# Kernel optimization log

Hardware: AMD Instinct MI355X
Metric: run time of the kernel (lower is better)

## Reference

```python
import jax, jax.numpy as jnp
import numpy as np

B, N, F, L = 8, 2048, 128, 2
SLOPE = 0.1  # LeakyReLU negative slope

def lrelu(v):
    return jnp.where(v >= 0, v, SLOPE * v)

def setup_inputs() -> dict:
    key = jax.random.key(0)
    ks = jax.random.split(key, 7)
    scale = 1.0 / np.sqrt(F)
    return {
        "x": jax.random.normal(ks[0], (B, N, F), dtype=jnp.float32),
        "W3": jax.random.normal(ks[1], (L, F, F), dtype=jnp.float32) * scale,
        "b3": jnp.zeros((L, F), dtype=jnp.float32),
        "W4": jax.random.normal(ks[2], (L, F, F), dtype=jnp.float32) * scale,
        "b4": jnp.zeros((L, F), dtype=jnp.float32),
        "W5": jax.random.normal(ks[3], (L, F, F), dtype=jnp.float32) * scale,
        "b5": jnp.zeros((L, F), dtype=jnp.float32),
    }

def reference(x, W3, b3, W4, b4, W5, b5):
    # GraphStack of L GraphLayer modules, mes_type '0':
    #   weight_ij = dot(LeakyReLU(g3(n_i)), LeakyReLU(g4(n_j)))
    #   message_i = mean_{j != i} weight_ij * n_j
    #   n_i_out   = LeakyReLU(g5(message_i)) + n_i
    n = x.shape[1]
    for l in range(W3.shape[0]):
        w1 = lrelu(jnp.einsum('bnf,fg->bng', x, W3[l]) + b3[l])  # [B,N,F]
        w2 = lrelu(jnp.einsum('bnf,fg->bng', x, W4[l]) + b4[l])  # [B,N,F]
        wt = jnp.einsum('bif,bjf->bij', w1, w2)                  # pairwise weights [B,N,N]
        diag = jnp.einsum('bif,bif->bi', w1, w2)                 # self weights to exclude
        msg = (jnp.einsum('bij,bjf->bif', wt, x) - diag[..., None] * x) / (n - 1)
        x = lrelu(jnp.einsum('bif,fg->big', msg, W5[l]) + b5[l]) + x
    return x
```

## Files before the change

### kernel.cpp

```cpp
#include <hip/hip_runtime.h>

#define BB 8
#define NN 2048
#define FF 128
#define NL 2
#define SLOPE 0.1f
#define NROW (BB * NN)
#define XS_STRIDE 136

typedef __attribute__((ext_vector_type(8))) short short8;
typedef __attribute__((ext_vector_type(4))) float f32x4;

__device__ __forceinline__ float lrelu(float v) { return v >= 0.f ? v : SLOPE * v; }

__device__ __forceinline__ ushort f2bf(float f) {
    uint u = __float_as_uint(f);
    return (ushort)((u + 0x7fffu + ((u >> 16) & 1u)) >> 16);
}

__global__ __launch_bounds__(256) void k_prep(
    const float* __restrict__ W3, const float* __restrict__ W4,
    const float* __restrict__ W5, ushort* __restrict__ Wt)
{
    const int idx = blockIdx.x * 256 + threadIdx.x;
    const int m = idx >> 14;
    const int rem = idx & 16383;
    const int f = rem & 127;
    const int g = rem >> 7;
    const int l = m / 3, w = m % 3;
    const float* src = (w == 0) ? W3 : (w == 1) ? W4 : W5;
    Wt[m * 16384 + g * 128 + f] = f2bf(src[l * 16384 + f * 128 + g]);
}

__global__ __launch_bounds__(512) void k_w12(
    const float* __restrict__ x, const ushort* __restrict__ w3t,
    const ushort* __restrict__ w4t, const float* __restrict__ b3,
    const float* __restrict__ b4, ushort* __restrict__ w1b,
    ushort* __restrict__ w2t, ushort* __restrict__ xt,
    float* __restrict__ diag)
{
    __shared__ ushort xs[64 * XS_STRIDE];
    __shared__ float diag_s[64];

    const int tid = threadIdx.x;
    const int row0 = blockIdx.x * 64;
    const int b = row0 >> 11;
    const int jloc0 = row0 & 2047;

    if (tid < 64) diag_s[tid] = 0.f;

    const float4* xg4 = (const float4*)(x + (size_t)row0 * FF);
#pragma unroll
    for (int i = 0; i < 4; i++) {
        const int f4 = i * 512 + tid;
        const int row = f4 >> 5;
        const int k = (f4 & 31) * 4;
        float4 v = xg4[f4];
        ushort4 h;
        h.x = f2bf(v.x); h.y = f2bf(v.y); h.z = f2bf(v.z); h.w = f2bf(v.w);
        *(ushort4*)&xs[row * XS_STRIDE + k] = h;
    }
    __syncthreads();

    {
        const int g = tid >> 2;
        const int h = tid & 3;
        uint p[8];
#pragma unroll
        for (int jj = 0; jj < 8; jj++) {
            const uint lo = xs[(h * 16 + jj * 2) * XS_STRIDE + g];
            const uint hi = xs[(h * 16 + jj * 2 + 1) * XS_STRIDE + g];
            p[jj] = lo | (hi << 16);
        }
        uint4* dst = (uint4*)&xt[(size_t)b * (FF * NN) + (size_t)g * NN + jloc0 + h * 16];
        dst[0] = make_uint4(p[0], p[1], p[2], p[3]);
        dst[1] = make_uint4(p[4], p[5], p[6], p[7]);
    }

    const int lane = tid & 63;
    const int wave = tid >> 6;
    const int c = lane & 15;
    const int quad = lane >> 4;
    const int n = wave * 16 + c;

    f32x4 acc1[4], acc2[4];
#pragma unroll
    for (int rt = 0; rt < 4; rt++) { acc1[rt] = (f32x4)0.f; acc2[rt] = (f32x4)0.f; }

#pragma unroll
    for (int kk = 0; kk < 4; kk++) {
        short8 bf3 = *(const short8*)&w3t[n * 128 + kk * 32 + quad * 8];
        short8 bf4 = *(const short8*)&w4t[n * 128 + kk * 32 + quad * 8];
#pragma unroll
        for (int rt = 0; rt < 4; rt++) {
            short8 a = *(const short8*)&xs[(rt * 16 + c) * XS_STRIDE + kk * 32 + quad * 8];
            acc1[rt] = __builtin_amdgcn_mfma_f32_16x16x32_bf16(a, bf3, acc1[rt], 0, 0, 0);
            acc2[rt] = __builtin_amdgcn_mfma_f32_16x16x32_bf16(a, bf4, acc2[rt], 0, 0, 0);
        }
    }

    const int gcol = wave * 16 + c;
    const float bb3 = b3[gcol], bb4 = b4[gcol];
    float dpar[4][4];

#pragma unroll
    for (int rt = 0; rt < 4; rt++) {
        ushort w2p[4];
#pragma unroll
        for (int r = 0; r < 4; r++) {
            const float v1 = lrelu(acc1[rt][r] + bb3);
            const float v2 = lrelu(acc2[rt][r] + bb4);
            const int grow = row0 + rt * 16 + quad * 4 + r;
            w1b[(size_t)grow * FF + gcol] = f2bf(v1);
            w2p[r] = f2bf(v2);
            dpar[rt][r] = v1 * v2;
        }
        const uint lo = (uint)w2p[0] | ((uint)w2p[1] << 16);
        const uint hi = (uint)w2p[2] | ((uint)w2p[3] << 16);
        uint2* dst = (uint2*)&w2t[(size_t)b * (FF * NN) + (size_t)gcol * NN +
                                  jloc0 + rt * 16 + quad * 4];
        *dst = make_uint2(lo, hi);
    }

#pragma unroll
    for (int rt = 0; rt < 4; rt++) {
#pragma unroll
        for (int r = 0; r < 4; r++) {
            float dp = dpar[rt][r];
            dp += __shfl_xor(dp, 1, 64);
            dp += __shfl_xor(dp, 2, 64);
            dp += __shfl_xor(dp, 4, 64);
            dp += __shfl_xor(dp, 8, 64);
            if (c == 0) atomicAdd(&diag_s[rt * 16 + quad * 4 + r], dp);
        }
    }
    __syncthreads();
    if (tid < 64) diag[row0 + tid] = diag_s[tid];
}

__global__ __launch_bounds__(256) void k_S2(
    const ushort* __restrict__ xt, const ushort* __restrict__ w2t,
    ushort* __restrict__ St)
{
    __shared__ float red[4][512];
    const int tid = threadIdx.x;
    const int lane = tid & 63;
    const int wave = tid >> 6;
    const int c = lane & 15;
    const int quad = lane >> 4;

    const int b  = blockIdx.x >> 5;
    const int gq = (blockIdx.x >> 3) & 3;
    const int fs = blockIdx.x & 7;

    const ushort* xtb = xt + (size_t)b * (FF * NN);
    const ushort* w2b = w2t + (size_t)b * (FF * NN);

    const int j0 = wave * 512 + quad * 8;
    const ushort* a0p = &xtb[(gq * 32 + c) * NN + j0];
    const ushort* a1p = &xtb[(gq * 32 + 16 + c) * NN + j0];
    const ushort* bp  = &w2b[(fs * 16 + c) * NN + j0];

    f32x4 acc0 = (f32x4)0.f, acc1 = (f32x4)0.f;
#pragma unroll
    for (int it = 0; it < 16; it++) {
        short8 a0 = *(const short8*)(a0p + it * 32);
        short8 a1 = *(const short8*)(a1p + it * 32);
        short8 bf = *(const short8*)(bp + it * 32);
        acc0 = __builtin_amdgcn_mfma_f32_16x16x32_bf16(a0, bf, acc0, 0, 0, 0);
        acc1 = __builtin_amdgcn_mfma_f32_16x16x32_bf16(a1, bf, acc1, 0, 0, 0);
    }

#pragma unroll
    for (int r = 0; r < 4; r++) {
        red[wave][(quad * 4 + r) * 16 + c] = acc0[r];
        red[wave][(16 + quad * 4 + r) * 16 + c] = acc1[r];
    }
    __syncthreads();

#pragma unroll
    for (int i = 0; i < 2; i++) {
        const int idx = i * 256 + tid;
        const float s = red[0][idx] + red[1][idx] + red[2][idx] + red[3][idx];
        const int gl = idx >> 4;
        const int fl = idx & 15;
        St[(size_t)b * (FF * FF) + (size_t)(gq * 32 + gl) * FF + fs * 16 + fl] = f2bf(s);
    }
}

__global__ __launch_bounds__(512) void k_out(
    const float* __restrict__ x, const ushort* __restrict__ w1b,
    const ushort* __restrict__ St, const float* __restrict__ diag,
    const ushort* __restrict__ w5t, const float* __restrict__ b5,
    float* __restrict__ out)
{
    __shared__ ushort w1s[64 * XS_STRIDE];
    __shared__ ushort ms[64 * XS_STRIDE];

    const int tid = threadIdx.x;
    const int row0 = blockIdx.x * 64;
    const int b = row0 >> 11;
    const ushort* Sb = St + (size_t)b * (FF * FF);

#pragma unroll
    for (int i = 0; i < 2; i++) {
        const int off = (i * 512 + tid) * 8;
        const int row = off >> 7;
        const int k = off & 127;
        short8 v = *(const short8*)&w1b[(size_t)row0 * FF + off];
        *(short8*)&w1s[row * XS_STRIDE + k] = v;
    }
    __syncthreads();

    const int lane = tid & 63;
    const int wave = tid >> 6;
    const int c = lane & 15;
    const int quad = lane >> 4;
    const int n = wave * 16 + c;

    f32x4 accm[4];
#pragma unroll
    for (int rt = 0; rt < 4; rt++) accm[rt] = (f32x4)0.f;

#pragma unroll
    for (int kk = 0; kk < 4; kk++) {
        short8 bf = *(const short8*)&Sb[n * 128 + kk * 32 + quad * 8];
#pragma unroll
        for (int rt = 0; rt < 4; rt++) {
            short8 a = *(const short8*)&w1s[(rt * 16 + c) * XS_STRIDE + kk * 32 + quad * 8];
            accm[rt] = __builtin_amdgcn_mfma_f32_16x16x32_bf16(a, bf, accm[rt], 0, 0, 0);
        }
    }

    const float inv = 1.f / (float)(NN - 1);
    const int gcol = wave * 16 + c;
    float xsv[4][4];
#pragma unroll
    for (int rt = 0; rt < 4; rt++) {
        float dg[4];
#pragma unroll
        for (int r = 0; r < 4; r++) dg[r] = diag[row0 + rt * 16 + quad * 4 + r];
#pragma unroll
        for (int r = 0; r < 4; r++) {
            const int lrow = rt * 16 + quad * 4 + r;
            const float xv = x[(size_t)(row0 + lrow) * FF + gcol];
            xsv[rt][r] = xv;
            const float m = (accm[rt][r] - dg[r] * xv) * inv;
            ms[lrow * XS_STRIDE + gcol] = f2bf(m);
        }
    }
    __syncthreads();

    f32x4 acc2[4];
#pragma unroll
    for (int rt = 0; rt < 4; rt++) acc2[rt] = (f32x4)0.f;

#pragma unroll
    for (int kk = 0; kk < 4; kk++) {
        short8 bf = *(const short8*)&w5t[n * 128 + kk * 32 + quad * 8];
#pragma unroll
        for (int rt = 0; rt < 4; rt++) {
            short8 a = *(const short8*)&ms[(rt * 16 + c) * XS_STRIDE + kk * 32 + quad * 8];
            acc2[rt] = __builtin_amdgcn_mfma_f32_16x16x32_bf16(a, bf, acc2[rt], 0, 0, 0);
        }
    }

    const float bb = b5[gcol];
#pragma unroll
    for (int rt = 0; rt < 4; rt++) {
#pragma unroll
        for (int r = 0; r < 4; r++) {
            const int grow = row0 + rt * 16 + quad * 4 + r;
            out[(size_t)grow * FF + gcol] = lrelu(acc2[rt][r] + bb) + xsv[rt][r];
        }
    }
}

__global__ __launch_bounds__(512) void k_out_w12(
    const float* __restrict__ x, const ushort* __restrict__ w1b_in,
    const ushort* __restrict__ St, const float* __restrict__ diag_in,
    const ushort* __restrict__ w5t, const float* __restrict__ b5,
    float* __restrict__ out,
    const ushort* __restrict__ w3t, const ushort* __restrict__ w4t,
    const float* __restrict__ b3, const float* __restrict__ b4,
    ushort* __restrict__ w1b, ushort* __restrict__ w2t,
    ushort* __restrict__ xt, float* __restrict__ diag)
{
    __shared__ ushort sA[64 * XS_STRIDE];
    __shared__ ushort sB[64 * XS_STRIDE];
    __shared__ float diag_s[64];

    const int tid = threadIdx.x;
    const int row0 = blockIdx.x * 64;
    const int b = row0 >> 11;
    const int jloc0 = row0 & 2047;
    const ushort* Sb = St + (size_t)b * (FF * FF);

    if (tid < 64) diag_s[tid] = 0.f;

#pragma unroll
    for (int i = 0; i < 2; i++) {
        const int off = (i * 512 + tid) * 8;
        const int row = off >> 7;
        const int k = off & 127;
        short8 v = *(const short8*)&w1b_in[(size_t)row0 * FF + off];
        *(short8*)&sA[row * XS_STRIDE + k] = v;
    }
    __syncthreads();

    const int lane = tid & 63;
    const int wave = tid >> 6;
    const int c = lane & 15;
    const int quad = lane >> 4;
    const int n = wave * 16 + c;
    const int gcol = wave * 16 + c;

    f32x4 accm[4];
#pragma unroll
    for (int rt = 0; rt < 4; rt++) accm[rt] = (f32x4)0.f;

#pragma unroll
    for (int kk = 0; kk < 4; kk++) {
        short8 bf = *(const short8*)&Sb[n * 128 + kk * 32 + quad * 8];
#pragma unroll
        for (int rt = 0; rt < 4; rt++) {
            short8 a = *(const short8*)&sA[(rt * 16 + c) * XS_STRIDE + kk * 32 + quad * 8];
            accm[rt] = __builtin_amdgcn_mfma_f32_16x16x32_bf16(a, bf, accm[rt], 0, 0, 0);
        }
    }

    const float inv = 1.f / (float)(NN - 1);
    float xsv[4][4];
#pragma unroll
    for (int rt = 0; rt < 4; rt++) {
        float dg[4];
#pragma unroll
        for (int r = 0; r < 4; r++) dg[r] = diag_in[row0 + rt * 16 + quad * 4 + r];
#pragma unroll
        for (int r = 0; r < 4; r++) {
            const int lrow = rt * 16 + quad * 4 + r;
            const float xv = x[(size_t)(row0 + lrow) * FF + gcol];
            xsv[rt][r] = xv;
            const float m = (accm[rt][r] - dg[r] * xv) * inv;
            sB[lrow * XS_STRIDE + gcol] = f2bf(m);
        }
    }
    __syncthreads();

    f32x4 acc2[4];
#pragma unroll
    for (int rt = 0; rt < 4; rt++) acc2[rt] = (f32x4)0.f;

#pragma unroll
    for (int kk = 0; kk < 4; kk++) {
        short8 bf = *(const short8*)&w5t[n * 128 + kk * 32 + quad * 8];
#pragma unroll
        for (int rt = 0; rt < 4; rt++) {
            short8 a = *(const short8*)&sB[(rt * 16 + c) * XS_STRIDE + kk * 32 + quad * 8];
            acc2[rt] = __builtin_amdgcn_mfma_f32_16x16x32_bf16(a, bf, acc2[rt], 0, 0, 0);
        }
    }

    const float bb = b5[gcol];
#pragma unroll
    for (int rt = 0; rt < 4; rt++) {
#pragma unroll
        for (int r = 0; r < 4; r++) {
            const int lrow = rt * 16 + quad * 4 + r;
            const float ov = lrelu(acc2[rt][r] + bb) + xsv[rt][r];
            out[(size_t)(row0 + lrow) * FF + gcol] = ov;
            sA[lrow * XS_STRIDE + gcol] = f2bf(ov);
        }
    }
    __syncthreads();

    {
        const int g = tid >> 2;
        const int h = tid & 3;
        uint p[8];
#pragma unroll
        for (int jj = 0; jj < 8; jj++) {
            const uint lo = sA[(h * 16 + jj * 2) * XS_STRIDE + g];
            const uint hi = sA[(h * 16 + jj * 2 + 1) * XS_STRIDE + g];
            p[jj] = lo | (hi << 16);
        }
        uint4* dst = (uint4*)&xt[(size_t)b * (FF * NN) + (size_t)g * NN + jloc0 + h * 16];
        dst[0] = make_uint4(p[0], p[1], p[2], p[3]);
        dst[1] = make_uint4(p[4], p[5], p[6], p[7]);
    }

    f32x4 acc1n[4], acc2n[4];
#pragma unroll
    for (int rt = 0; rt < 4; rt++) { acc1n[rt] = (f32x4)0.f; acc2n[rt] = (f32x4)0.f; }

#pragma unroll
    for (int kk = 0; kk < 4; kk++) {
        short8 bf3 = *(const short8*)&w3t[n * 128 + kk * 32 + quad * 8];
        short8 bf4 = *(const short8*)&w4t[n * 128 + kk * 32 + quad * 8];
#pragma unroll
        for (int rt = 0; rt < 4; rt++) {
            short8 a = *(const short8*)&sA[(rt * 16 + c) * XS_STRIDE + kk * 32 + quad * 8];
            acc1n[rt] = __builtin_amdgcn_mfma_f32_16x16x32_bf16(a, bf3, acc1n[rt], 0, 0, 0);
            acc2n[rt] = __builtin_amdgcn_mfma_f32_16x16x32_bf16(a, bf4, acc2n[rt], 0, 0, 0);
        }
    }

    const float bb3 = b3[gcol], bb4 = b4[gcol];
    float dpar[4][4];
#pragma unroll
    for (int rt = 0; rt < 4; rt++) {
        ushort w2p[4];
#pragma unroll
        for (int r = 0; r < 4; r++) {
            const float v1 = lrelu(acc1n[rt][r] + bb3);
            const float v2 = lrelu(acc2n[rt][r] + bb4);
            const int grow = row0 + rt * 16 + quad * 4 + r;
            w1b[(size_t)grow * FF + gcol] = f2bf(v1);
            w2p[r] = f2bf(v2);
            dpar[rt][r] = v1 * v2;
        }
        const uint lo = (uint)w2p[0] | ((uint)w2p[1] << 16);
        const uint hi = (uint)w2p[2] | ((uint)w2p[3] << 16);
        uint2* dst = (uint2*)&w2t[(size_t)b * (FF * NN) + (size_t)gcol * NN +
                                  jloc0 + rt * 16 + quad * 4];
        *dst = make_uint2(lo, hi);
    }

#pragma unroll
    for (int rt = 0; rt < 4; rt++) {
#pragma unroll
        for (int r = 0; r < 4; r++) {
            float dp = dpar[rt][r];
            dp += __shfl_xor(dp, 1, 64);
            dp += __shfl_xor(dp, 2, 64);
            dp += __shfl_xor(dp, 4, 64);
            dp += __shfl_xor(dp, 8, 64);
            if (c == 0) atomicAdd(&diag_s[rt * 16 + quad * 4 + r], dp);
        }
    }
    __syncthreads();
    if (tid < 64) diag[row0 + tid] = diag_s[tid];
}

extern "C" void kernel_launch(void* const* d_in, const int* in_sizes, int n_in,
                              void* d_out, int out_size, void* d_ws, size_t ws_size,
                              hipStream_t stream)
{
    const float* x  = (const float*)d_in[0];
    const float* W3 = (const float*)d_in[1];
    const float* b3 = (const float*)d_in[2];
    const float* W4 = (const float*)d_in[3];
    const float* b4 = (const float*)d_in[4];
    const float* W5 = (const float*)d_in[5];
    const float* b5 = (const float*)d_in[6];
    float* out = (float*)d_out;

    char* ws = (char*)d_ws;
    ushort* w1b   = (ushort*)(ws);
    ushort* w2t   = (ushort*)(ws + ((size_t)4  << 20));
    ushort* xt    = (ushort*)(ws + ((size_t)8  << 20));
    float*  diag  = (float*) (ws + ((size_t)12 << 20));
    ushort* St    = (ushort*)(ws + ((size_t)13 << 20));
    ushort* Wt    = (ushort*)(ws + ((size_t)14 << 20));

    const ushort* w3t0 = Wt;
    const ushort* w4t0 = Wt + 16384;
    const ushort* w5t0 = Wt + 2 * 16384;
    const ushort* w3t1 = Wt + 3 * 16384;
    const ushort* w4t1 = Wt + 4 * 16384;
    const ushort* w5t1 = Wt + 5 * 16384;

    const int rowBlocks = NROW / 64;

    k_prep<<<384, 256, 0, stream>>>(W3, W4, W5, Wt);

    k_w12<<<rowBlocks, 512, 0, stream>>>(x, w3t0, w4t0, b3, b4, w1b, w2t, xt, diag);
    k_S2<<<256, 256, 0, stream>>>(xt, w2t, St);
    k_out_w12<<<rowBlocks, 512, 0, stream>>>(x, w1b, St, diag, w5t0, b5, out,
                                             w3t1, w4t1, b3 + FF, b4 + FF,
                                             w1b, w2t, xt, diag);
    k_S2<<<256, 256, 0, stream>>>(xt, w2t, St);
    k_out<<<rowBlocks, 512, 0, stream>>>(out, w1b, St, diag, w5t1, b5 + FF, out);
}
```

Measured before the change: 120.6 us.

## Fuse weight transpose/bf16 conversion into consumer kernels via LDS staging

Removes the separate k_prep launch. Each row-block kernel now converts and transposes the fp32 weights into shared memory itself. Weight B-fragments are read from LDS instead of global memory. The k_S2 block index mapping is also changed so the batch index varies fastest. In exchange, every one of the 256 blocks redoes the 128x128 transpose-convert work with strided global reads, and LDS use per block rises to roughly 70-105 KB, which limits occupancy.

After: 118.1 us. 2.1% less time.

```diff
diff --git a/kernel.cpp b/kernel.cpp
--- a/kernel.cpp
+++ b/kernel.cpp
@@ -1,12 +1,10 @@
 #include <hip/hip_runtime.h>
 
-#define BB 8
 #define NN 2048
 #define FF 128
-#define NL 2
 #define SLOPE 0.1f
-#define NROW (BB * NN)
-#define XS_STRIDE 136
+#define WSTR 136
+#define TSTR 136
 
 typedef __attribute__((ext_vector_type(8))) short short8;
 typedef __attribute__((ext_vector_type(4))) float f32x4;
@@ -18,28 +16,29 @@
     return (ushort)((u + 0x7fffu + ((u >> 16) & 1u)) >> 16);
 }
 
-__global__ __launch_bounds__(256) void k_prep(
-    const float* __restrict__ W3, const float* __restrict__ W4,
-    const float* __restrict__ W5, ushort* __restrict__ Wt)
+__device__ __forceinline__ void wtrans(const float* __restrict__ W, ushort* wl, int tid) {
+#pragma unroll
+    for (int u = 0; u < 4; u++) {
+        const int g = tid & 127;
+        const int fgrp = (tid >> 7) + u * 4;
+        short8 v;
+#pragma unroll
+        for (int j = 0; j < 8; j++) v[j] = (short)f2bf(W[(fgrp * 8 + j) * 128 + g]);
+        *(short8*)&wl[g * WSTR + fgrp * 8] = v;
+    }
+}
+
+__global__ __launch_bounds__(512) void k_w12(
+    const float* __restrict__ x,
+    const float* __restrict__ W3, const float* __restrict__ b3,
+    const float* __restrict__ W4, const float* __restrict__ b4,
+    ushort* __restrict__ w1b, ushort* __restrict__ w2t,
+    ushort* __restrict__ xt, float* __restrict__ diag)
 {
-    const int idx = blockIdx.x * 256 + threadIdx.x;
-    const int m = idx >> 14;
-    const int rem = idx & 16383;
-    const int f = rem & 127;
-    const int g = rem >> 7;
-    const int l = m / 3, w = m % 3;
-    const float* src = (w == 0) ? W3 : (w == 1) ? W4 : W5;
-    Wt[m * 16384 + g * 128 + f] = f2bf(src[l * 16384 + f * 128 + g]);
-}
-
-__global__ __launch_bounds__(512) void k_w12(
-    const float* __restrict__ x, const ushort* __restrict__ w3t,
-    const ushort* __restrict__ w4t, const float* __restrict__ b3,
-    const float* __restrict__ b4, ushort* __restrict__ w1b,
-    ushort* __restrict__ w2t, ushort* __restrict__ xt,
-    float* __restrict__ diag)
-{
-    __shared__ ushort xs[64 * XS_STRIDE];
+    __shared__ __align__(16) char smem[87040];
+    ushort* xs = (ushort*)smem;
+    ushort* wA = (ushort*)(smem + 17408);
+    ushort* wB = (ushort*)(smem + 52224);
     __shared__ float diag_s[64];
 
     const int tid = threadIdx.x;
@@ -58,8 +57,10 @@
         float4 v = xg4[f4];
         ushort4 h;
         h.x = f2bf(v.x); h.y = f2bf(v.y); h.z = f2bf(v.z); h.w = f2bf(v.w);
-        *(ushort4*)&xs[row * XS_STRIDE + k] = h;
-    }
+        *(ushort4*)&xs[row * TSTR + k] = h;
+    }
+    wtrans(W3, wA, tid);
+    wtrans(W4, wB, tid);
     __syncthreads();
 
     {
@@ -68,8 +69,8 @@
         uint p[8];
 #pragma unroll
         for (int jj = 0; jj < 8; jj++) {
-            const uint lo = xs[(h * 16 + jj * 2) * XS_STRIDE + g];
-            const uint hi = xs[(h * 16 + jj * 2 + 1) * XS_STRIDE + g];
+            const uint lo = xs[(h * 16 + jj * 2) * TSTR + g];
+            const uint hi = xs[(h * 16 + jj * 2 + 1) * TSTR + g];
             p[jj] = lo | (hi << 16);
         }
         uint4* dst = (uint4*)&xt[(size_t)b * (FF * NN) + (size_t)g * NN + jloc0 + h * 16];
@@ -81,7 +82,7 @@
     const int wave = tid >> 6;
     const int c = lane & 15;
     const int quad = lane >> 4;
-    const int n = wave * 16 + c;
+    const int gcol = wave * 16 + c;
 
     f32x4 acc1[4], acc2[4];
 #pragma unroll
@@ -89,20 +90,18 @@
 
 #pragma unroll
     for (int kk = 0; kk < 4; kk++) {
-        short8 bf3 = *(const short8*)&w3t[n * 128 + kk * 32 + quad * 8];
-        short8 bf4 = *(const short8*)&w4t[n * 128 + kk * 32 + quad * 8];
-#pragma unroll
-        for (int rt = 0; rt < 4; rt++) {
-            short8 a = *(const short8*)&xs[(rt * 16 + c) * XS_STRIDE + kk * 32 + quad * 8];
+        short8 bf3 = *(const short8*)&wA[gcol * WSTR + kk * 32 + quad * 8];
+        short8 bf4 = *(const short8*)&wB[gcol * WSTR + kk * 32 + quad * 8];
+#pragma unroll
+        for (int rt = 0; rt < 4; rt++) {
+            short8 a = *(const short8*)&xs[(rt * 16 + c) * TSTR + kk * 32 + quad * 8];
             acc1[rt] = __builtin_amdgcn_mfma_f32_16x16x32_bf16(a, bf3, acc1[rt], 0, 0, 0);
             acc2[rt] = __builtin_amdgcn_mfma_f32_16x16x32_bf16(a, bf4, acc2[rt], 0, 0, 0);
         }
     }
 
-    const int gcol = wave * 16 + c;
     const float bb3 = b3[gcol], bb4 = b4[gcol];
     float dpar[4][4];
-
 #pragma unroll
     for (int rt = 0; rt < 4; rt++) {
         ushort w2p[4];
@@ -149,9 +148,10 @@
     const int c = lane & 15;
     const int quad = lane >> 4;
 
-    const int b  = blockIdx.x >> 5;
-    const int gq = (blockIdx.x >> 3) & 3;
-    const int fs = blockIdx.x & 7;
+    const int b     = blockIdx.x & 7;
+    const int slice = blockIdx.x >> 3;
+    const int gq    = slice >> 3;
+    const int fs    = slice & 7;
 
     const ushort* xtb = xt + (size_t)b * (FF * NN);
     const ushort* w2b = w2t + (size_t)b * (FF * NN);
@@ -188,106 +188,21 @@
     }
 }
 
-__global__ __launch_bounds__(512) void k_out(
-    const float* __restrict__ x, const ushort* __restrict__ w1b,
-    const ushort* __restrict__ St, const float* __restrict__ diag,
-    const ushort* __restrict__ w5t, const float* __restrict__ b5,
-    float* __restrict__ out)
-{
-    __shared__ ushort w1s[64 * XS_STRIDE];
-    __shared__ ushort ms[64 * XS_STRIDE];
-
-    const int tid = threadIdx.x;
-    const int row0 = blockIdx.x * 64;
-    const int b = row0 >> 11;
-    const ushort* Sb = St + (size_t)b * (FF * FF);
-
-#pragma unroll
-    for (int i = 0; i < 2; i++) {
-        const int off = (i * 512 + tid) * 8;
-        const int row = off >> 7;
-        const int k = off & 127;
-        short8 v = *(const short8*)&w1b[(size_t)row0 * FF + off];
-        *(short8*)&w1s[row * XS_STRIDE + k] = v;
-    }
-    __syncthreads();
-
-    const int lane = tid & 63;
-    const int wave = tid >> 6;
-    const int c = lane & 15;
-    const int quad = lane >> 4;
-    const int n = wave * 16 + c;
-
-    f32x4 accm[4];
-#pragma unroll
-    for (int rt = 0; rt < 4; rt++) accm[rt] = (f32x4)0.f;
-
-#pragma unroll
-    for (int kk = 0; kk < 4; kk++) {
-        short8 bf = *(const short8*)&Sb[n * 128 + kk * 32 + quad * 8];
-#pragma unroll
-        for (int rt = 0; rt < 4; rt++) {
-            short8 a = *(const short8*)&w1s[(rt * 16 + c) * XS_STRIDE + kk * 32 + quad * 8];
-            accm[rt] = __builtin_amdgcn_mfma_f32_16x16x32_bf16(a, bf, accm[rt], 0, 0, 0);
-        }
-    }
-
-    const float inv = 1.f / (float)(NN - 1);
-    const int gcol = wave * 16 + c;
-    float xsv[4][4];
-#pragma unroll
-    for (int rt = 0; rt < 4; rt++) {
-        float dg[4];
-#pragma unroll
-        for (int r = 0; r < 4; r++) dg[r] = diag[row0 + rt * 16 + quad * 4 + r];
-#pragma unroll
-        for (int r = 0; r < 4; r++) {
-            const int lrow = rt * 16 + quad * 4 + r;
-            const float xv = x[(size_t)(row0 + lrow) * FF + gcol];
-            xsv[rt][r] = xv;
-            const float m = (accm[rt][r] - dg[r] * xv) * inv;
-            ms[lrow * XS_STRIDE + gcol] = f2bf(m);
-        }
-    }
-    __syncthreads();
-
-    f32x4 acc2[4];
-#pragma unroll
-    for (int rt = 0; rt < 4; rt++) acc2[rt] = (f32x4)0.f;
-
-#pragma unroll
-    for (int kk = 0; kk < 4; kk++) {
-        short8 bf = *(const short8*)&w5t[n * 128 + kk * 32 + quad * 8];
-#pragma unroll
-        for (int rt = 0; rt < 4; rt++) {
-            short8 a = *(const short8*)&ms[(rt * 16 + c) * XS_STRIDE + kk * 32 + quad * 8];
-            acc2[rt] = __builtin_amdgcn_mfma_f32_16x16x32_bf16(a, bf, acc2[rt], 0, 0, 0);
-        }
-    }
-
-    const float bb = b5[gcol];
-#pragma unroll
-    for (int rt = 0; rt < 4; rt++) {
-#pragma unroll
-        for (int r = 0; r < 4; r++) {
-            const int grow = row0 + rt * 16 + quad * 4 + r;
-            out[(size_t)grow * FF + gcol] = lrelu(acc2[rt][r] + bb) + xsv[rt][r];
-        }
-    }
-}
-
 __global__ __launch_bounds__(512) void k_out_w12(
     const float* __restrict__ x, const ushort* __restrict__ w1b_in,
     const ushort* __restrict__ St, const float* __restrict__ diag_in,
-    const ushort* __restrict__ w5t, const float* __restrict__ b5,
+    const float* __restrict__ W5, const float* __restrict__ b5,
     float* __restrict__ out,
-    const ushort* __restrict__ w3t, const ushort* __restrict__ w4t,
-    const float* __restrict__ b3, const float* __restrict__ b4,
+    const float* __restrict__ W3n, const float* __restrict__ b3n,
+    const float* __restrict__ W4n, const float* __restrict__ b4n,
     ushort* __restrict__ w1b, ushort* __restrict__ w2t,
     ushort* __restrict__ xt, float* __restrict__ diag)
 {
-    __shared__ ushort sA[64 * XS_STRIDE];
-    __shared__ ushort sB[64 * XS_STRIDE];
+    __shared__ __align__(16) char smem[104448];
+    ushort* sA = (ushort*)smem;
+    ushort* sB = (ushort*)(smem + 17408);
+    ushort* wA = (ushort*)(smem + 34816);
+    ushort* wB = (ushort*)(smem + 69632);
     __shared__ float diag_s[64];
 
     const int tid = threadIdx.x;
@@ -304,15 +219,15 @@
         const int row = off >> 7;
         const int k = off & 127;
         short8 v = *(const short8*)&w1b_in[(size_t)row0 * FF + off];
-        *(short8*)&sA[row * XS_STRIDE + k] = v;
-    }
+        *(short8*)&sA[row * TSTR + k] = v;
+    }
+    wtrans(W5, wA, tid);
     __syncthreads();
 
     const int lane = tid & 63;
     const int wave = tid >> 6;
     const int c = lane & 15;
     const int quad = lane >> 4;
-    const int n = wave * 16 + c;
     const int gcol = wave * 16 + c;
 
     f32x4 accm[4];
@@ -321,10 +236,10 @@
 
 #pragma unroll
     for (int kk = 0; kk < 4; kk++) {
-        short8 bf = *(const short8*)&Sb[n * 128 + kk * 32 + quad * 8];
-#pragma unroll
-        for (int rt = 0; rt < 4; rt++) {
-            short8 a = *(const short8*)&sA[(rt * 16 + c) * XS_STRIDE + kk * 32 + quad * 8];
+        short8 bf = *(const short8*)&Sb[gcol * 128 + kk * 32 + quad * 8];
+#pragma unroll
+        for (int rt = 0; rt < 4; rt++) {
+            short8 a = *(const short8*)&sA[(rt * 16 + c) * TSTR + kk * 32 + quad * 8];
             accm[rt] = __builtin_amdgcn_mfma_f32_16x16x32_bf16(a, bf, accm[rt], 0, 0, 0);
         }
     }
@@ -342,7 +257,7 @@
             const float xv = x[(size_t)(row0 + lrow) * FF + gcol];
             xsv[rt][r] = xv;
             const float m = (accm[rt][r] - dg[r] * xv) * inv;
-            sB[lrow * XS_STRIDE + gcol] = f2bf(m);
+            sB[lrow * TSTR + gcol] = f2bf(m);
         }
     }
     __syncthreads();
@@ -353,10 +268,10 @@
 
 #pragma unroll
     for (int kk = 0; kk < 4; kk++) {
-        short8 bf = *(const short8*)&w5t[n * 128 + kk * 32 + quad * 8];
-#pragma unroll
-        for (int rt = 0; rt < 4; rt++) {
-            short8 a = *(const short8*)&sB[(rt * 16 + c) * XS_STRIDE + kk * 32 + quad * 8];
+        short8 bf = *(const short8*)&wA[gcol * WSTR + kk * 32 + quad * 8];
+#pragma unroll
+        for (int rt = 0; rt < 4; rt++) {
+            short8 a = *(const short8*)&sB[(rt * 16 + c) * TSTR + kk * 32 + quad * 8];
             acc2[rt] = __builtin_amdgcn_mfma_f32_16x16x32_bf16(a, bf, acc2[rt], 0, 0, 0);
         }
     }
@@ -369,25 +284,28 @@
             const int lrow = rt * 16 + quad * 4 + r;
             const float ov = lrelu(acc2[rt][r] + bb) + xsv[rt][r];
             out[(size_t)(row0 + lrow) * FF + gcol] = ov;
-            sA[lrow * XS_STRIDE + gcol] = f2bf(ov);
-        }
-    }
-    __syncthreads();
-
+            sA[lrow * TSTR + gcol] = f2bf(ov);
+        }
+    }
+    __syncthreads();
+
+    wtrans(W3n, wA, tid);
+    wtrans(W4n, wB, tid);
     {
         const int g = tid >> 2;
         const int h = tid & 3;
         uint p[8];
 #pragma unroll
         for (int jj = 0; jj < 8; jj++) {
-            const uint lo = sA[(h * 16 + jj * 2) * XS_STRIDE + g];
-            const uint hi = sA[(h * 16 + jj * 2 + 1) * XS_STRIDE + g];
+            const uint lo = sA[(h * 16 + jj * 2) * TSTR + g];
+            const uint hi = sA[(h * 16 + jj * 2 + 1) * TSTR + g];
             p[jj] = lo | (hi << 16);
         }
         uint4* dst = (uint4*)&xt[(size_t)b * (FF * NN) + (size_t)g * NN + jloc0 + h * 16];
         dst[0] = make_uint4(p[0], p[1], p[2], p[3]);
         dst[1] = make_uint4(p[4], p[5], p[6], p[7]);
     }
+    __syncthreads();
 
     f32x4 acc1n[4], acc2n[4];
 #pragma unroll
@@ -395,17 +313,17 @@
 
 #pragma unroll
     for (int kk = 0; kk < 4; kk++) {
-        short8 bf3 = *(const short8*)&w3t[n * 128 + kk * 32 + quad * 8];
-        short8 bf4 = *(const short8*)&w4t[n * 128 + kk * 32 + quad * 8];
-#pragma unroll
-        for (int rt = 0; rt < 4; rt++) {
-            short8 a = *(const short8*)&sA[(rt * 16 + c) * XS_STRIDE + kk * 32 + quad * 8];
+        short8 bf3 = *(const short8*)&wA[gcol * WSTR + kk * 32 + quad * 8];
+        short8 bf4 = *(const short8*)&wB[gcol * WSTR + kk * 32 + quad * 8];
+#pragma unroll
+        for (int rt = 0; rt < 4; rt++) {
+            short8 a = *(const short8*)&sA[(rt * 16 + c) * TSTR + kk * 32 + quad * 8];
             acc1n[rt] = __builtin_amdgcn_mfma_f32_16x16x32_bf16(a, bf3, acc1n[rt], 0, 0, 0);
             acc2n[rt] = __builtin_amdgcn_mfma_f32_16x16x32_bf16(a, bf4, acc2n[rt], 0, 0, 0);
         }
     }
 
-    const float bb3 = b3[gcol], bb4 = b4[gcol];
+    const float bb3 = b3n[gcol], bb4 = b4n[gcol];
     float dpar[4][4];
 #pragma unroll
     for (int rt = 0; rt < 4; rt++) {
@@ -440,6 +358,96 @@
     }
     __syncthreads();
     if (tid < 64) diag[row0 + tid] = diag_s[tid];
+}
+
+__global__ __launch_bounds__(512) void k_out(
+    const float* __restrict__ xres, const ushort* __restrict__ w1b,
+    const ushort* __restrict__ St, const float* __restrict__ diag,
+    const float* __restrict__ W5n, const float* __restrict__ b5n,
+    float* __restrict__ out)
+{
+    __shared__ __align__(16) char smem[69632];
+    ushort* w1s = (ushort*)smem;
+    ushort* ms  = (ushort*)(smem + 17408);
+    ushort* wA  = (ushort*)(smem + 34816);
+
+    const int tid = threadIdx.x;
+    const int row0 = blockIdx.x * 64;
+    const int b = row0 >> 11;
+    const ushort* Sb = St + (size_t)b * (FF * FF);
+
+#pragma unroll
+    for (int i = 0; i < 2; i++) {
+        const int off = (i * 512 + tid) * 8;
+        const int row = off >> 7;
+        const int k = off & 127;
+        short8 v = *(const short8*)&w1b[(size_t)row0 * FF + off];
+        *(short8*)&w1s[row * TSTR + k] = v;
+    }
+    wtrans(W5n, wA, tid);
+    __syncthreads();
+
+    const int lane = tid & 63;
+    const int wave = tid >> 6;
+    const int c = lane & 15;
+    const int quad = lane >> 4;
+    const int gcol = wave * 16 + c;
+
+    f32x4 accm[4];
+#pragma unroll
+    for (int rt = 0; rt < 4; rt++) accm[rt] = (f32x4)0.f;
+
+#pragma unroll
+    for (int kk = 0; kk < 4; kk++) {
+        short8 bf = *(const short8*)&Sb[gcol * 128 + kk * 32 + quad * 8];
+#pragma unroll
+        for (int rt = 0; rt < 4; rt++) {
+            short8 a = *(const short8*)&w1s[(rt * 16 + c) * TSTR + kk * 32 + quad * 8];
+            accm[rt] = __builtin_amdgcn_mfma_f32_16x16x32_bf16(a, bf, accm[rt], 0, 0, 0);
+        }
+    }
+
+    const float inv = 1.f / (float)(NN - 1);
+    float xsv[4][4];
+#pragma unroll
+    for (int rt = 0; rt < 4; rt++) {
+        float dg[4];
+#pragma unroll
+        for (int r = 0; r < 4; r++) dg[r] = diag[row0 + rt * 16 + quad * 4 + r];
+#pragma unroll
+        for (int r = 0; r < 4; r++) {
+            const int lrow = rt * 16 + quad * 4 + r;
+            const float xv = xres[(size_t)(row0 + lrow) * FF + gcol];
+            xsv[rt][r] = xv;
+            const float m = (accm[rt][r] - dg[r] * xv) * inv;
+            ms[lrow * TSTR + gcol] = f2bf(m);
+        }
+    }
+    __syncthreads();
+
+    f32x4 acc2[4];
+#pragma unroll
+    for (int rt = 0; rt < 4; rt++) acc2[rt] = (f32x4)0.f;
+
+#pragma unroll
+    for (int kk = 0; kk < 4; kk++) {
+        short8 bf = *(const short8*)&wA[gcol * WSTR + kk * 32 + quad * 8];
+#pragma unroll
+        for (int rt = 0; rt < 4; rt++) {
+            short8 a = *(const short8*)&ms[(rt * 16 + c) * TSTR + kk * 32 + quad * 8];
+            acc2[rt] = __builtin_amdgcn_mfma_f32_16x16x32_bf16(a, bf, acc2[rt], 0, 0, 0);
+        }
+    }
+
+    const float bb = b5n[gcol];
+#pragma unroll
+    for (int rt = 0; rt < 4; rt++) {
+#pragma unroll
+        for (int r = 0; r < 4; r++) {
+            const int grow = row0 + rt * 16 + quad * 4 + r;
+            out[(size_t)grow * FF + gcol] = lrelu(acc2[rt][r] + bb) + xsv[rt][r];
+        }
+    }
 }
 
 extern "C" void kernel_launch(void* const* d_in, const int* in_sizes, int n_in,
@@ -456,29 +464,17 @@
     float* out = (float*)d_out;
 
     char* ws = (char*)d_ws;
-    ushort* w1b   = (ushort*)(ws);
-    ushort* w2t   = (ushort*)(ws + ((size_t)4  << 20));
-    ushort* xt    = (ushort*)(ws + ((size_t)8  << 20));
-    float*  diag  = (float*) (ws + ((size_t)12 << 20));
-    ushort* St    = (ushort*)(ws + ((size_t)13 << 20));
-    ushort* Wt    = (ushort*)(ws + ((size_t)14 << 20));
-
-    const ushort* w3t0 = Wt;
-    const ushort* w4t0 = Wt + 16384;
-    const ushort* w5t0 = Wt + 2 * 16384;
-    const ushort* w3t1 = Wt + 3 * 16384;
-    const ushort* w4t1 = Wt + 4 * 16384;
-    const ushort* w5t1 = Wt + 5 * 16384;
-
-    const int rowBlocks = NROW / 64;
-
-    k_prep<<<384, 256, 0, stream>>>(W3, W4, W5, Wt);
-
-    k_w12<<<rowBlocks, 512, 0, stream>>>(x, w3t0, w4t0, b3, b4, w1b, w2t, xt, diag);
+    ushort* w1b  = (ushort*)(ws);
+    ushort* w2t  = (ushort*)(ws + ((size_t)4  << 20));
+    ushort* xt   = (ushort*)(ws + ((size_t)8  << 20));
+    float*  diag = (float*) (ws + ((size_t)12 << 20));
+    ushort* St   = (ushort*)(ws + ((size_t)13 << 20));
+
+    k_w12<<<256, 512, 0, stream>>>(x, W3, b3, W4, b4, w1b, w2t, xt, diag);
     k_S2<<<256, 256, 0, stream>>>(xt, w2t, St);
-    k_out_w12<<<rowBlocks, 512, 0, stream>>>(x, w1b, St, diag, w5t0, b5, out,
-                                             w3t1, w4t1, b3 + FF, b4 + FF,
-                                             w1b, w2t, xt, diag);
+    k_out_w12<<<256, 512, 0, stream>>>(x, w1b, St, diag, W5, b5, out,
+                                       W3 + 16384, b3 + FF, W4 + 16384, b4 + FF,
+                                       w1b, w2t, xt, diag);
     k_S2<<<256, 256, 0, stream>>>(xt, w2t, St);
-    k_out<<<rowBlocks, 512, 0, stream>>>(out, w1b, St, diag, w5t1, b5 + FF, out);
-}
+    k_out<<<256, 512, 0, stream>>>(out, w1b, St, diag, W5 + 16384, b5 + FF, out);
+}
```
